# Optimization experiments

Hardware: AMD Instinct MI355X
Metric: run time of the kernel (lower is better)

The kernel has to match this reference:

```python
import jax, jax.numpy as jnp
import numpy as np

N = 50000      # nodes
E = 800000     # edges (avg degree 16)
F_IN = 128     # num_features
H = 64         # hidden_dim
G = 64         # graphs in batch


def setup_inputs() -> dict:
    key = jax.random.key(0)
    ks = jax.random.split(key, 20)
    inp = {
        "x": jax.random.normal(ks[0], (N, F_IN), jnp.float32),
        "edge_index": jax.random.randint(ks[1], (2, E), 0, N, dtype=jnp.int32).astype(jnp.int64),
        "batch": jnp.sort(jax.random.randint(ks[2], (N,), 0, G, dtype=jnp.int32)).astype(jnp.int64),
    }
    # GraphConv layer dims: in -> out
    dims = [(F_IN, H), (H, 2 * H), (2 * H, 3 * H), (3 * H, H)]
    k = 3
    for i, (din, dout) in enumerate(dims):
        s = 1.0 / np.sqrt(din).astype(np.float32)
        inp[f"w{i+1}_rel"] = jax.random.normal(ks[k], (din, dout), jnp.float32) * s
        inp[f"w{i+1}_root"] = jax.random.normal(ks[k + 1], (din, dout), jnp.float32) * s
        inp[f"b{i+1}"] = jnp.zeros((dout,), jnp.float32)
        k += 2
    inp["head_w"] = jax.random.normal(ks[k], (H, 1), jnp.float32) * (1.0 / np.sqrt(H).astype(np.float32))
    inp["head_b"] = jnp.zeros((1,), jnp.float32)
    return inp


def _graph_conv(x, src, dst, w_rel, w_root, b):
    # PyG GraphConv: out = lin_rel(sum_{j in N(i)} x_j) + lin_root(x_i)
    agg = jax.ops.segment_sum(x[src], dst, num_segments=N)  # [N, din]
    return agg @ w_rel + b + x @ w_root


def reference(x, edge_index, batch,
              w1_rel, w1_root, b1,
              w2_rel, w2_root, b2,
              w3_rel, w3_root, b3,
              w4_rel, w4_root, b4,
              head_w, head_b):
    src, dst = edge_index[0], edge_index[1]
    h = jax.nn.relu(_graph_conv(x, src, dst, w1_rel, w1_root, b1))
    h = jax.nn.relu(_graph_conv(h, src, dst, w2_rel, w2_root, b2))
    h = jax.nn.relu(_graph_conv(h, src, dst, w3_rel, w3_root, b3))
    h = _graph_conv(h, src, dst, w4_rel, w4_root, b4)          # [N, H]
    # global_mean_pool over graph ids
    sums = jax.ops.segment_sum(h, batch, num_segments=G)       # [G, H]
    counts = jax.ops.segment_sum(jnp.ones((N,), h.dtype), batch, num_segments=G)
    pooled = sums / jnp.maximum(counts, 1.0)[:, None]          # [G, H]
    return pooled @ head_w + head_b                            # [G, 1]
```

## Files before the change

kernel.cpp:

```cpp
#include <hip/hip_runtime.h>


#define NNODES 50000
#define NEDGES 800000
#define NGRAPH 64
#define NBUK 256
#define BSZ 196
#define EPB (NEDGES / NBUK)
#define CVT_NB (NNODES * 128 / 4 / 256)
#define PACK_NB (160 * 512 / 256)
#define RGRID ((NNODES + 127) / 128)
#define RCHUNK ((RGRID + 7) / 8)

typedef __attribute__((ext_vector_type(8))) __bf16 bf16x8;
typedef __attribute__((ext_vector_type(16))) float f32x16;

__device__ __forceinline__ unsigned short f2bf(float f) {
    unsigned u = __float_as_uint(f);
    u += 0x7fff + ((u >> 16) & 1);
    return (unsigned short)(u >> 16);
}
__device__ __forceinline__ float bf2f(unsigned b) {
    return __uint_as_float(b << 16);
}


__global__ void hist_kernel(const int* __restrict__ dst, int* __restrict__ cnt) {
    __shared__ int h[NBUK];
    int tid = threadIdx.x, k = blockIdx.x;
    h[tid] = 0;
    __syncthreads();
    int end = (k + 1) * EPB;
    for (int i = k * EPB + tid; i < end; i += 256)
        atomicAdd(&h[dst[i] / BSZ], 1);
    __syncthreads();
    cnt[tid * NBUK + k] = h[tid];
}

__global__ void scan1_kernel(int* __restrict__ a, int* __restrict__ bsum, int n) {
    __shared__ int buf[256];
    int tid = threadIdx.x;
    int i = blockIdx.x * 256 + tid;
    int v = (i < n) ? a[i] : 0;
    buf[tid] = v;
    __syncthreads();
    #pragma unroll
    for (int off = 1; off < 256; off <<= 1) {
        int t = (tid >= off) ? buf[tid - off] : 0;
        __syncthreads();
        buf[tid] += t;
        __syncthreads();
    }
    if (i < n) a[i] = buf[tid] - v;
    if (tid == 255) bsum[blockIdx.x] = buf[255];
}

__global__ void scan2_kernel(int* __restrict__ bsum, int nb) {
    __shared__ int buf[256];
    int tid = threadIdx.x;
    int v = (tid < nb) ? bsum[tid] : 0;
    buf[tid] = v;
    __syncthreads();
    #pragma unroll
    for (int off = 1; off < 256; off <<= 1) {
        int t = (tid >= off) ? buf[tid - off] : 0;
        __syncthreads();
        buf[tid] += t;
        __syncthreads();
    }
    if (tid < nb) bsum[tid] = buf[tid] - v;
}

__global__ void partition_kernel(const int* __restrict__ src, const int* __restrict__ dst,
                                 const int* __restrict__ cnt, const int* __restrict__ bsum,
                                 unsigned long long* __restrict__ pedge) {
    __shared__ int lbase[NBUK];
    int tid = threadIdx.x, k = blockIdx.x;
    lbase[tid] = cnt[tid * NBUK + k] + bsum[tid];
    __syncthreads();
    int end = (k + 1) * EPB;
    for (int i = k * EPB + tid; i < end; i += 256) {
        int s = src[i], d = dst[i];
        int pos = atomicAdd(&lbase[d / BSZ], 1);
        pedge[pos] = (unsigned long long)(unsigned)s | ((unsigned long long)(unsigned)d << 32);
    }
}

__global__ void build_kernel(const unsigned long long* __restrict__ pedge,
                             const int* __restrict__ bsum,
                             int* __restrict__ rp, int* __restrict__ csr) {
    __shared__ int sdeg[256], sc[256], sbase[256], sfill[256];
    int tid = threadIdx.x, b = blockIdx.x;
    int node0 = b * BSZ;
    int ncnt = NNODES - node0;
    if (ncnt > BSZ) ncnt = BSZ;
    if (ncnt < 0) ncnt = 0;
    int seg0 = bsum[b];
    int seg1 = (b + 1 < NBUK) ? bsum[b + 1] : NEDGES;
    sdeg[tid] = 0;
    sfill[tid] = 0;
    __syncthreads();
    for (int i = seg0 + tid; i < seg1; i += 256)
        atomicAdd(&sdeg[(int)(pedge[i] >> 32) - node0], 1);
    __syncthreads();
    sc[tid] = sdeg[tid];
    __syncthreads();
    #pragma unroll
    for (int off = 1; off < 256; off <<= 1) {
        int t = (tid >= off) ? sc[tid - off] : 0;
        __syncthreads();
        sc[tid] += t;
        __syncthreads();
    }
    sbase[tid] = sc[tid] - sdeg[tid];
    if (tid < ncnt) rp[node0 + tid] = seg0 + sbase[tid];
    if (b == NBUK - 1 && tid == 0) rp[NNODES] = NEDGES;
    __syncthreads();
    for (int i = seg0 + tid; i < seg1; i += 256) {
        unsigned long long p = pedge[i];
        int d = (int)(p >> 32) - node0;
        int pos = atomicAdd(&sfill[d], 1);
        csr[seg0 + sbase[d] + pos] = (int)(p & 0xffffffffu);
    }
}


__device__ __forceinline__ void pack32(const float* __restrict__ W, unsigned short* __restrict__ dst,
                                       int KS_tot, int ks0, int dcols, int ct0,
                                       int tl, int ksl, int lane, int j) {
    int k = ksl * 16 + ((lane >> 5) << 3) + j;
    int col = tl * 32 + (lane & 31);
    dst[(((size_t)(ct0 + tl) * KS_tot + (ks0 + ksl)) * 64 + lane) * 8 + j] = f2bf(W[k * dcols + col]);
}

__global__ void prep_kernel(const float* __restrict__ x, unsigned short* __restrict__ xbf,
                            const float* __restrict__ w1_rel, const float* __restrict__ w1_root,
                            const float* __restrict__ w2_rel, const float* __restrict__ w2_root,
                            const float* __restrict__ w3_rel, const float* __restrict__ w3_root,
                            unsigned short* __restrict__ pL1, unsigned short* __restrict__ pL2,
                            unsigned short* __restrict__ pL3,
                            const float* __restrict__ w4_rel, const float* __restrict__ w4_root,
                            const float* __restrict__ b4, const float* __restrict__ head_w,
                            float* __restrict__ wr, float* __restrict__ wt,
                            float* __restrict__ cbuf) {
    int b = blockIdx.x;
    int tid = threadIdx.x;
    if (b < CVT_NB) {
        int i = b * 256 + tid;
        float4 v = ((const float4*)x)[i];
        unsigned lo = (unsigned)f2bf(v.x) | ((unsigned)f2bf(v.y) << 16);
        unsigned hi = (unsigned)f2bf(v.z) | ((unsigned)f2bf(v.w) << 16);
        ((uint2*)xbf)[i] = make_uint2(lo, hi);
    } else if (b < CVT_NB + PACK_NB) {
        int idx = (b - CVT_NB) * 256 + tid;
        int g = idx >> 9;
        int t = idx & 511;
        int lane = (t >> 3) & 63, j = t & 7;
        if (g < 16)       { int gl = g;       pack32(w1_rel,  pL1, 8,  0, 64,  0, gl / 8, gl % 8, lane, j); }
        else if (g < 32)  { int gl = g - 16;  pack32(w1_root, pL1, 8,  0, 64,  2, gl / 8, gl % 8, lane, j); }
        else if (g < 48)  { int gl = g - 32;  pack32(w2_rel,  pL2, 8,  0, 128, 0, gl / 4, gl % 4, lane, j); }
        else if (g < 64)  { int gl = g - 48;  pack32(w2_root, pL2, 8,  4, 128, 0, gl / 4, gl % 4, lane, j); }
        else if (g < 112) { int gl = g - 64;  pack32(w3_rel,  pL3, 16, 0, 192, 0, gl / 8, gl % 8, lane, j); }
        else              { int gl = g - 112; pack32(w3_root, pL3, 16, 8, 192, 0, gl / 8, gl % 8, lane, j); }
    } else {
        if (tid < 192) {
            float ar = 0.f, at = 0.f;
            for (int j = 0; j < 64; j++) {
                float hw = head_w[j];
                ar = fmaf(w4_rel[tid * 64 + j], hw, ar);
                at = fmaf(w4_root[tid * 64 + j], hw, at);
            }
            wr[tid] = ar;
            wt[tid] = at;
        } else if (tid == 192) {
            float c = 0.f;
            for (int j = 0; j < 64; j++) c = fmaf(b4[j], head_w[j], c);
            cbuf[0] = c;
        }
    }
}


template<int KS, int NC, int ST>
__global__ __launch_bounds__(256, 4) void gemm_v4(
    const unsigned short* __restrict__ A, const unsigned short* __restrict__ W,
    const float* __restrict__ bias, unsigned short* __restrict__ OUT,
    int ldo, int ocol0, int relu, int N,
    const float* __restrict__ wrp, const float* __restrict__ wtp,
    float* __restrict__ sb, float* __restrict__ tb)
{
    const int K = KS * 16;
    int i = blockIdx.x;
    int chunk = i / (NC * 8);
    int rem = i - chunk * (NC * 8);
    int cg = rem >> 3;
    int rowb = chunk * 8 + (rem & 7);
    int tid = threadIdx.x;
    int wave = tid >> 6, lane = tid & 63;
    int l32 = lane & 31, half = lane >> 5;
    int rbase = rowb * 128 + wave * 32;
    if (rbase >= N) return;

    int arow = rbase + l32;
    if (arow >= N) arow = N - 1;
    const unsigned short* ap = A + (size_t)arow * K + half * 8;
    const unsigned short* wp = W + (size_t)cg * KS * 512 + lane * 8;

    f32x16 acc;
    #pragma unroll
    for (int r = 0; r < 16; r++) acc[r] = 0.f;

    #pragma unroll 1
    for (int kb = 0; kb < KS; kb += 8) {
        bf16x8 areg[8], breg[8];
        #pragma unroll
        for (int j = 0; j < 8; j++) {
            areg[j] = *(const bf16x8*)(ap + (kb + j) * 16);
            breg[j] = *(const bf16x8*)(wp + (size_t)(kb + j) * 512);
        }
        #pragma unroll
        for (int j = 0; j < 8; j++)
            acc = __builtin_amdgcn_mfma_f32_32x32x16_bf16(areg[j], breg[j], acc, 0, 0, 0);
    }

    int col = cg * 32 + l32;
    float bi = bias ? bias[col] : 0.f;
    if constexpr (ST) {
        float wrv = wrp[col], wtv = wtp[col];
        #pragma unroll
        for (int reg = 0; reg < 16; reg++) {
            int row = rbase + (reg & 3) + 8 * (reg >> 2) + 4 * half;
            float v = fmaxf(acc[reg] + bi, 0.f);
            float sv = v * wrv;
            float tv = v * wtv;
            #pragma unroll
            for (int m = 1; m < 32; m <<= 1) {
                sv += __shfl_xor(sv, m, 64);
                tv += __shfl_xor(tv, m, 64);
            }
            if (l32 == 0 && row < N) {
                atomicAdd(&sb[row], sv);
                atomicAdd(&tb[row], tv);
            }
        }
    } else {
        #pragma unroll
        for (int reg = 0; reg < 16; reg++) {
            int row = rbase + (reg & 3) + 8 * (reg >> 2) + 4 * half;
            if (row < N) {
                float v = acc[reg] + bi;
                if (relu) v = fmaxf(v, 0.f);
                OUT[(size_t)row * ldo + ocol0 + col] = f2bf(v);
            }
        }
    }
}


__device__ __forceinline__ void acc8(float* a, uint4 u) {
    a[0] += bf2f(u.x & 0xffffu); a[1] += bf2f(u.x >> 16);
    a[2] += bf2f(u.y & 0xffffu); a[3] += bf2f(u.y >> 16);
    a[4] += bf2f(u.z & 0xffffu); a[5] += bf2f(u.z >> 16);
    a[6] += bf2f(u.w & 0xffffu); a[7] += bf2f(u.w >> 16);
}

template<int LPF, int SUBS>
__global__ void agg_kernel_v3(const unsigned short* __restrict__ X, int ldx,
                              const int* __restrict__ rp, const int* __restrict__ csr,
                              const unsigned short* __restrict__ root, int ldr,
                              const float* __restrict__ bias, int relu,
                              unsigned short* __restrict__ OUT, int ldo, int N) {
    int t = blockIdx.x * blockDim.x + threadIdx.x;
    int node = t / (SUBS * LPF);
    int r = t % (SUBS * LPF);
    int sub = r / LPF;
    int sl = r % LPF;
    if (node >= N) return;
    float a[8] = {0.f, 0.f, 0.f, 0.f, 0.f, 0.f, 0.f, 0.f};
    int e0 = rp[node], e1 = rp[node + 1];
    const unsigned short* xb = X + 8 * sl;
    int e = e0 + sub;
    for (; e + SUBS < e1; e += 2 * SUBS) {
        int s0 = csr[e], s1 = csr[e + SUBS];
        uint4 u0 = *(const uint4*)(xb + (size_t)s0 * ldx);
        uint4 u1 = *(const uint4*)(xb + (size_t)s1 * ldx);
        acc8(a, u0);
        acc8(a, u1);
    }
    if (e < e1) {
        uint4 u = *(const uint4*)(xb + (size_t)csr[e] * ldx);
        acc8(a, u);
    }
    #pragma unroll
    for (int m = LPF; m < SUBS * LPF; m <<= 1)
        #pragma unroll
        for (int i = 0; i < 8; i++) a[i] += __shfl_xor(a[i], m, 64);
    if (sub == 0) {
        if (root) {
            uint4 u = *(const uint4*)(root + (size_t)node * ldr + 8 * sl);
            acc8(a, u);
        }
        if (bias) {
            float4 b0 = *(const float4*)(bias + 8 * sl);
            float4 b1 = *(const float4*)(bias + 8 * sl + 4);
            a[0] += b0.x; a[1] += b0.y; a[2] += b0.z; a[3] += b0.w;
            a[4] += b1.x; a[5] += b1.y; a[6] += b1.z; a[7] += b1.w;
        }
        if (relu) {
            #pragma unroll
            for (int i = 0; i < 8; i++) a[i] = fmaxf(a[i], 0.f);
        }
        uint4 o;
        o.x = (unsigned)f2bf(a[0]) | ((unsigned)f2bf(a[1]) << 16);
        o.y = (unsigned)f2bf(a[2]) | ((unsigned)f2bf(a[3]) << 16);
        o.z = (unsigned)f2bf(a[4]) | ((unsigned)f2bf(a[5]) << 16);
        o.w = (unsigned)f2bf(a[6]) | ((unsigned)f2bf(a[7]) << 16);
        *(uint4*)(OUT + (size_t)node * ldo + 8 * sl) = o;
    }
}


__global__ void aggpool_kernel(const float* __restrict__ s, const float* __restrict__ t,
                               const int* __restrict__ rp, const int* __restrict__ csr,
                               const int* __restrict__ batch, float* __restrict__ gsum,
                               int* __restrict__ cnt, int* __restrict__ done,
                               const float* __restrict__ cbuf, const float* __restrict__ head_b,
                               float* __restrict__ out, int N) {
    __shared__ float ls[NGRAPH];
    __shared__ int lc[NGRAPH];
    __shared__ int lastflag;
    int tid = threadIdx.x;
    if (tid < NGRAPH) { ls[tid] = 0.f; lc[tid] = 0; }
    __syncthreads();
    int gidx = blockIdx.x * blockDim.x + tid;
    int node = gidx >> 2, sub = gidx & 3;
    if (node < N) {
        float a = 0.f;
        int e = rp[node] + sub, e1 = rp[node + 1];
        for (; e + 4 < e1; e += 8) a += s[csr[e]] + s[csr[e + 4]];
        if (e < e1) a += s[csr[e]];
        a += __shfl_xor(a, 1, 64);
        a += __shfl_xor(a, 2, 64);
        if (sub == 0) {
            int g = batch[node];
            atomicAdd(&ls[g], a + t[node]);
            atomicAdd(&lc[g], 1);
        }
    }
    __syncthreads();
    if (tid < NGRAPH && lc[tid] > 0) {
        atomicAdd(&gsum[tid], ls[tid]);
        atomicAdd(&cnt[tid], lc[tid]);
    }
    __syncthreads();
    if (tid == 0) {
        __threadfence();
        int d = atomicAdd(done, 1);
        lastflag = (d == (int)gridDim.x - 1);
    }
    __syncthreads();
    if (lastflag && tid < NGRAPH) {
        __threadfence();
        float gs = atomicAdd(&gsum[tid], 0.0f);
        int c = atomicAdd(&cnt[tid], 0);
        float cc = (float)(c > 0 ? c : 1);
        out[tid] = gs / cc + cbuf[0] + head_b[0];
    }
}


extern "C" void kernel_launch(void* const* d_in, const int* in_sizes, int n_in,
                              void* d_out, int out_size, void* d_ws, size_t ws_size,
                              hipStream_t stream) {
    const float* x       = (const float*)d_in[0];
    const int*   edge    = (const int*)d_in[1];
    const int*   batch   = (const int*)d_in[2];
    const float* w1_rel  = (const float*)d_in[3];
    const float* w1_root = (const float*)d_in[4];
    const float* b1      = (const float*)d_in[5];
    const float* w2_rel  = (const float*)d_in[6];
    const float* w2_root = (const float*)d_in[7];
    const float* b2      = (const float*)d_in[8];
    const float* w3_rel  = (const float*)d_in[9];
    const float* w3_root = (const float*)d_in[10];
    const float* b3      = (const float*)d_in[11];
    const float* w4_rel  = (const float*)d_in[12];
    const float* w4_root = (const float*)d_in[13];
    const float* b4      = (const float*)d_in[14];
    const float* head_w  = (const float*)d_in[15];
    const float* head_b  = (const float*)d_in[16];
    float* out = (float*)d_out;

    const int N = NNODES, E = NEDGES;
    const int* src = edge;
    const int* dst = edge + E;

    char* ws = (char*)d_ws;
    size_t off = 0;
    auto alloc = [&](size_t bytes) -> char* {
        char* p = ws + off;
        off = (off + bytes + 255) & ~(size_t)255;
        return p;
    };
    float* gsum  = (float*)alloc(NGRAPH * 4);
    int*   cnt   = (int*)alloc(NGRAPH * 4);
    int*   done  = (int*)alloc(4);
    float* sbuf  = (float*)alloc((size_t)N * 4);
    float* tbuf  = (float*)alloc((size_t)N * 4);
    size_t zero_bytes = off;
    int*   bcnt  = (int*)alloc((size_t)NBUK * NBUK * 4);
    int*   bsum  = (int*)alloc(256 * 4);
    int*   rp    = (int*)alloc((size_t)(N + 1) * 4);
    int*   csr   = (int*)alloc((size_t)E * 4);
    unsigned long long* pedge = (unsigned long long*)alloc((size_t)E * 8);
    unsigned short* xbf    = (unsigned short*)alloc((size_t)N * 128 * 2);
    unsigned short* z1     = (unsigned short*)alloc((size_t)N * 128 * 2);
    unsigned short* combo2 = (unsigned short*)alloc((size_t)N * 128 * 2);
    unsigned short* combo3 = (unsigned short*)alloc((size_t)N * 256 * 2);
    unsigned short* pL1    = (unsigned short*)alloc(4 * 8 * 512 * 2);
    unsigned short* pL2    = (unsigned short*)alloc(4 * 8 * 512 * 2);
    unsigned short* pL3    = (unsigned short*)alloc(6 * 16 * 512 * 2);
    float* wr    = (float*)alloc(192 * 4);
    float* wt    = (float*)alloc(192 * 4);
    float* cbuf  = (float*)alloc(4);
    (void)ws_size;

    hipMemsetAsync(gsum, 0, zero_bytes, stream);

    const int TB = 256;

    hist_kernel<<<NBUK, 256, 0, stream>>>(dst, bcnt);
    scan1_kernel<<<NBUK, 256, 0, stream>>>(bcnt, bsum, NBUK * NBUK);
    scan2_kernel<<<1, 256, 0, stream>>>(bsum, NBUK);
    partition_kernel<<<NBUK, 256, 0, stream>>>(src, dst, bcnt, bsum, pedge);
    build_kernel<<<NBUK, 256, 0, stream>>>(pedge, bsum, rp, csr);

    prep_kernel<<<CVT_NB + PACK_NB + 1, 256, 0, stream>>>(
        x, xbf, w1_rel, w1_root, w2_rel, w2_root, w3_rel, w3_root,
        pL1, pL2, pL3, w4_rel, w4_root, b4, head_w, wr, wt, cbuf);

    gemm_v4<8, 4, 0><<<RCHUNK * 8 * 4, 256, 0, stream>>>(xbf, pL1, nullptr, z1, 128, 0, 0, N,
                                                         nullptr, nullptr, nullptr, nullptr);
    agg_kernel_v3<8, 4><<<(N * 32 + TB - 1) / TB, TB, 0, stream>>>(z1, 128, rp, csr,
                                                                   z1 + 64, 128, b1, 1, combo2 + 64, 128, N);
    agg_kernel_v3<8, 4><<<(N * 32 + TB - 1) / TB, TB, 0, stream>>>(combo2 + 64, 128, rp, csr,
                                                                   nullptr, 0, nullptr, 0, combo2, 128, N);
    gemm_v4<8, 4, 0><<<RCHUNK * 8 * 4, 256, 0, stream>>>(combo2, pL2, b2, combo3, 256, 128, 1, N,
                                                         nullptr, nullptr, nullptr, nullptr);
    agg_kernel_v3<16, 4><<<(N * 64 + TB - 1) / TB, TB, 0, stream>>>(combo3 + 128, 256, rp, csr,
                                                                    nullptr, 0, nullptr, 0, combo3, 256, N);
    gemm_v4<16, 6, 1><<<RCHUNK * 8 * 6, 256, 0, stream>>>(combo3, pL3, b3, nullptr, 0, 0, 0, N,
                                                          wr, wt, sbuf, tbuf);

    aggpool_kernel<<<(N * 4 + TB - 1) / TB, TB, 0, stream>>>(sbuf, tbuf, rp, csr, batch,
                                                             gsum, cnt, done, cbuf, head_b, out, N);
}
```

Before: 288.3 us.

## Stage GEMM tiles in LDS via global_load_lds and retune aggregation kernels

Replaces the per-column-group GEMM with a kernel where each block computes all output column tiles (or half of them) for 128 rows. The block stages the A tile and the packed weights into LDS using direct global-to-LDS loads with an XOR swizzle. This cuts redundant A-row reads across column-group blocks. It also changes the aggregation sub-lane count from 4 to 2, makes the pooling kernel use one thread per node, and replaces the last-block completion flag with a separate final kernel. The trade-offs are higher LDS use, which may lower occupancy, and one extra launch; the A staging reads rows past N for the last block without clamping.

```diff
diff --git a/kernel.cpp b/kernel.cpp
--- a/kernel.cpp
+++ b/kernel.cpp
@@ -22,6 +22,12 @@
 }
 __device__ __forceinline__ float bf2f(unsigned b) {
     return __uint_as_float(b << 16);
+}
+
+__device__ __forceinline__ void dma16(const void* g, void* l) {
+    __builtin_amdgcn_global_load_lds(
+        (const __attribute__((address_space(1))) void*)g,
+        (__attribute__((address_space(3))) void*)l, 16, 0, 0);
 }
 
 
@@ -181,58 +187,84 @@
 }
 
 
-template<int KS, int NC, int ST>
-__global__ __launch_bounds__(256, 4) void gemm_v4(
-    const unsigned short* __restrict__ A, const unsigned short* __restrict__ W,
+template<int KS, int NT, int NHALF, int ST, int KCH>
+__global__ __launch_bounds__(256) void gemm_v5(
+    const unsigned short* __restrict__ A, const unsigned short* __restrict__ Wall,
     const float* __restrict__ bias, unsigned short* __restrict__ OUT,
     int ldo, int ocol0, int relu, int N,
     const float* __restrict__ wrp, const float* __restrict__ wtp,
     float* __restrict__ sb, float* __restrict__ tb)
 {
     const int K = KS * 16;
+    const int CPC = KCH * 2;
+    __shared__ __align__(16) unsigned short sB[NT * KS * 512];
+    __shared__ __align__(16) unsigned short sA[128 * KCH * 16];
+
     int i = blockIdx.x;
-    int chunk = i / (NC * 8);
-    int rem = i - chunk * (NC * 8);
-    int cg = rem >> 3;
+    int chunk = i / (8 * NHALF);
+    int rem = i - chunk * (8 * NHALF);
+    int halfsel = rem >> 3;
     int rowb = chunk * 8 + (rem & 7);
+    int rbase = rowb * 128;
+    if (rbase >= N) return;
+
     int tid = threadIdx.x;
     int wave = tid >> 6, lane = tid & 63;
     int l32 = lane & 31, half = lane >> 5;
-    int rbase = rowb * 128 + wave * 32;
-    if (rbase >= N) return;
-
-    int arow = rbase + l32;
-    if (arow >= N) arow = N - 1;
-    const unsigned short* ap = A + (size_t)arow * K + half * 8;
-    const unsigned short* wp = W + (size_t)cg * KS * 512 + lane * 8;
-
-    f32x16 acc;
-    #pragma unroll
-    for (int r = 0; r < 16; r++) acc[r] = 0.f;
-
-    #pragma unroll 1
-    for (int kb = 0; kb < KS; kb += 8) {
-        bf16x8 areg[8], breg[8];
-        #pragma unroll
-        for (int j = 0; j < 8; j++) {
-            areg[j] = *(const bf16x8*)(ap + (kb + j) * 16);
-            breg[j] = *(const bf16x8*)(wp + (size_t)(kb + j) * 512);
-        }
-        #pragma unroll
-        for (int j = 0; j < 8; j++)
-            acc = __builtin_amdgcn_mfma_f32_32x32x16_bf16(areg[j], breg[j], acc, 0, 0, 0);
-    }
-
-    int col = cg * 32 + l32;
-    float bi = bias ? bias[col] : 0.f;
+    const unsigned short* W = Wall + (size_t)halfsel * NT * KS * 512;
+
+    #pragma unroll
+    for (int j = 0; j < NT * KS * 64 / 256; j++) {
+        int p = j * 256 + wave * 64;
+        dma16(W + ((size_t)p + lane) * 8, sB + (size_t)p * 8);
+    }
+
+    f32x16 acc[NT];
+    #pragma unroll
+    for (int t = 0; t < NT; t++)
+        #pragma unroll
+        for (int r = 0; r < 16; r++) acc[t][r] = 0.f;
+
+    int lr = wave * 32 + l32;
+
+    for (int kb = 0; kb < KS; kb += KCH) {
+        if (kb > 0) __syncthreads();
+        #pragma unroll
+        for (int j = 0; j < 128 * CPC / 256; j++) {
+            int p = j * 256 + wave * 64 + lane;
+            int r = p / CPC;
+            int c = p - r * CPC;
+            int cg = c ^ (r & (CPC - 1));
+            dma16(A + (size_t)(rbase + r) * K + kb * 16 + cg * 8,
+                  sA + (size_t)(j * 256 + wave * 64) * 8);
+        }
+        __syncthreads();
+        #pragma unroll
+        for (int l = 0; l < KCH; l++) {
+            int cs = (l * 2 + half) ^ (lr & (CPC - 1));
+            bf16x8 a = *(const bf16x8*)(sA + (size_t)lr * (KCH * 16) + cs * 8);
+            int ks = kb + l;
+            #pragma unroll
+            for (int t = 0; t < NT; t++) {
+                bf16x8 b = *(const bf16x8*)(sB + ((size_t)(t * KS + ks) * 64 + lane) * 8);
+                acc[t] = __builtin_amdgcn_mfma_f32_32x32x16_bf16(a, b, acc[t], 0, 0, 0);
+            }
+        }
+    }
+
+    int wrbase = rbase + wave * 32;
     if constexpr (ST) {
-        float wrv = wrp[col], wtv = wtp[col];
         #pragma unroll
         for (int reg = 0; reg < 16; reg++) {
-            int row = rbase + (reg & 3) + 8 * (reg >> 2) + 4 * half;
-            float v = fmaxf(acc[reg] + bi, 0.f);
-            float sv = v * wrv;
-            float tv = v * wtv;
+            int row = wrbase + (reg & 3) + 8 * (reg >> 2) + 4 * half;
+            float sv = 0.f, tv = 0.f;
+            #pragma unroll
+            for (int t = 0; t < NT; t++) {
+                int col = halfsel * NT * 32 + t * 32 + l32;
+                float v = fmaxf(acc[t][reg] + bias[col], 0.f);
+                sv = fmaf(v, wrp[col], sv);
+                tv = fmaf(v, wtp[col], tv);
+            }
             #pragma unroll
             for (int m = 1; m < 32; m <<= 1) {
                 sv += __shfl_xor(sv, m, 64);
@@ -245,12 +277,17 @@
         }
     } else {
         #pragma unroll
-        for (int reg = 0; reg < 16; reg++) {
-            int row = rbase + (reg & 3) + 8 * (reg >> 2) + 4 * half;
-            if (row < N) {
-                float v = acc[reg] + bi;
-                if (relu) v = fmaxf(v, 0.f);
-                OUT[(size_t)row * ldo + ocol0 + col] = f2bf(v);
+        for (int t = 0; t < NT; t++) {
+            int col = t * 32 + l32;
+            float bi = bias ? bias[col] : 0.f;
+            #pragma unroll
+            for (int reg = 0; reg < 16; reg++) {
+                int row = wrbase + (reg & 3) + 8 * (reg >> 2) + 4 * half;
+                if (row < N) {
+                    float v = acc[t][reg] + bi;
+                    if (relu) v = fmaxf(v, 0.f);
+                    OUT[(size_t)row * ldo + ocol0 + col] = f2bf(v);
+                }
             }
         }
     }
@@ -323,48 +360,39 @@
 __global__ void aggpool_kernel(const float* __restrict__ s, const float* __restrict__ t,
                                const int* __restrict__ rp, const int* __restrict__ csr,
                                const int* __restrict__ batch, float* __restrict__ gsum,
-                               int* __restrict__ cnt, int* __restrict__ done,
-                               const float* __restrict__ cbuf, const float* __restrict__ head_b,
-                               float* __restrict__ out, int N) {
+                               int* __restrict__ cnt, int N) {
     __shared__ float ls[NGRAPH];
     __shared__ int lc[NGRAPH];
-    __shared__ int lastflag;
     int tid = threadIdx.x;
     if (tid < NGRAPH) { ls[tid] = 0.f; lc[tid] = 0; }
     __syncthreads();
-    int gidx = blockIdx.x * blockDim.x + tid;
-    int node = gidx >> 2, sub = gidx & 3;
-    if (node < N) {
+    int n = blockIdx.x * blockDim.x + tid;
+    if (n < N) {
         float a = 0.f;
-        int e = rp[node] + sub, e1 = rp[node + 1];
-        for (; e + 4 < e1; e += 8) a += s[csr[e]] + s[csr[e + 4]];
-        if (e < e1) a += s[csr[e]];
-        a += __shfl_xor(a, 1, 64);
-        a += __shfl_xor(a, 2, 64);
-        if (sub == 0) {
-            int g = batch[node];
-            atomicAdd(&ls[g], a + t[node]);
-            atomicAdd(&lc[g], 1);
-        }
+        int e = rp[n], e1 = rp[n + 1];
+        for (; e + 3 < e1; e += 4) {
+            int s0 = csr[e], s1 = csr[e + 1], s2 = csr[e + 2], s3 = csr[e + 3];
+            a += s[s0] + s[s1] + s[s2] + s[s3];
+        }
+        for (; e < e1; e++) a += s[csr[e]];
+        int g = batch[n];
+        atomicAdd(&ls[g], a + t[n]);
+        atomicAdd(&lc[g], 1);
     }
     __syncthreads();
     if (tid < NGRAPH && lc[tid] > 0) {
         atomicAdd(&gsum[tid], ls[tid]);
         atomicAdd(&cnt[tid], lc[tid]);
     }
-    __syncthreads();
-    if (tid == 0) {
-        __threadfence();
-        int d = atomicAdd(done, 1);
-        lastflag = (d == (int)gridDim.x - 1);
-    }
-    __syncthreads();
-    if (lastflag && tid < NGRAPH) {
-        __threadfence();
-        float gs = atomicAdd(&gsum[tid], 0.0f);
-        int c = atomicAdd(&cnt[tid], 0);
-        float cc = (float)(c > 0 ? c : 1);
-        out[tid] = gs / cc + cbuf[0] + head_b[0];
+}
+
+__global__ void final_kernel(const float* __restrict__ gsum, const int* __restrict__ cnt,
+                             const float* __restrict__ cbuf, const float* __restrict__ head_b,
+                             float* __restrict__ out) {
+    int g = threadIdx.x;
+    if (g < NGRAPH) {
+        float c = (float)(cnt[g] > 0 ? cnt[g] : 1);
+        out[g] = gsum[g] / c + cbuf[0] + head_b[0];
     }
 }
 
@@ -404,7 +432,6 @@
     };
     float* gsum  = (float*)alloc(NGRAPH * 4);
     int*   cnt   = (int*)alloc(NGRAPH * 4);
-    int*   done  = (int*)alloc(4);
     float* sbuf  = (float*)alloc((size_t)N * 4);
     float* tbuf  = (float*)alloc((size_t)N * 4);
     size_t zero_bytes = off;
@@ -439,19 +466,19 @@
         x, xbf, w1_rel, w1_root, w2_rel, w2_root, w3_rel, w3_root,
         pL1, pL2, pL3, w4_rel, w4_root, b4, head_w, wr, wt, cbuf);
 
-    gemm_v4<8, 4, 0><<<RCHUNK * 8 * 4, 256, 0, stream>>>(xbf, pL1, nullptr, z1, 128, 0, 0, N,
-                                                         nullptr, nullptr, nullptr, nullptr);
-    agg_kernel_v3<8, 4><<<(N * 32 + TB - 1) / TB, TB, 0, stream>>>(z1, 128, rp, csr,
+    gemm_v5<8, 4, 1, 0, 8><<<RCHUNK * 8, 256, 0, stream>>>(
+        xbf, pL1, nullptr, z1, 128, 0, 0, N, nullptr, nullptr, nullptr, nullptr);
+    agg_kernel_v3<8, 2><<<(N * 16 + TB - 1) / TB, TB, 0, stream>>>(z1, 128, rp, csr,
                                                                    z1 + 64, 128, b1, 1, combo2 + 64, 128, N);
-    agg_kernel_v3<8, 4><<<(N * 32 + TB - 1) / TB, TB, 0, stream>>>(combo2 + 64, 128, rp, csr,
+    agg_kernel_v3<8, 2><<<(N * 16 + TB - 1) / TB, TB, 0, stream>>>(combo2 + 64, 128, rp, csr,
                                                                    nullptr, 0, nullptr, 0, combo2, 128, N);
-    gemm_v4<8, 4, 0><<<RCHUNK * 8 * 4, 256, 0, stream>>>(combo2, pL2, b2, combo3, 256, 128, 1, N,
-                                                         nullptr, nullptr, nullptr, nullptr);
-    agg_kernel_v3<16, 4><<<(N * 64 + TB - 1) / TB, TB, 0, stream>>>(combo3 + 128, 256, rp, csr,
+    gemm_v5<8, 4, 1, 0, 8><<<RCHUNK * 8, 256, 0, stream>>>(
+        combo2, pL2, b2, combo3, 256, 128, 1, N, nullptr, nullptr, nullptr, nullptr);
+    agg_kernel_v3<16, 2><<<(N * 32 + TB - 1) / TB, TB, 0, stream>>>(combo3 + 128, 256, rp, csr,
                                                                     nullptr, 0, nullptr, 0, combo3, 256, N);
-    gemm_v4<16, 6, 1><<<RCHUNK * 8 * 6, 256, 0, stream>>>(combo3, pL3, b3, nullptr, 0, 0, 0, N,
-                                                          wr, wt, sbuf, tbuf);
-
-    aggpool_kernel<<<(N * 4 + TB - 1) / TB, TB, 0, stream>>>(sbuf, tbuf, rp, csr, batch,
-                                                             gsum, cnt, done, cbuf, head_b, out, N);
-}
+    gemm_v5<16, 3, 2, 1, 4><<<RCHUNK * 8 * 2, 256, 0, stream>>>(
+        combo3, pL3, b3, nullptr, 0, 0, 0, N, wr, wt, sbuf, tbuf);
+
+    aggpool_kernel<<<(N + TB - 1) / TB, TB, 0, stream>>>(sbuf, tbuf, rp, csr, batch, gsum, cnt, N);
+    final_kernel<<<1, 64, 0, stream>>>(gsum, cnt, cbuf, head_b, out);
+}
```

Result: faster. 251.3 us (-12.8%).
